# Performance work log

Hardware: AMD Instinct MI355X
Metric: run time of the kernel (lower is better)

Reference implementation:

```python
import jax, jax.numpy as jnp
import numpy as np


def _fft_feats(x):
    # x: [B, 3, H, W] float32
    B, C, H, W = x.shape
    gray = 0.299 * x[:, 0] + 0.587 * x[:, 1] + 0.114 * x[:, 2]  # [B,H,W]
    mag = jnp.abs(jnp.fft.fftshift(jnp.fft.fft2(gray), axes=(-2, -1))) + 1e-8
    mag = mag / (mag.max(axis=(-2, -1), keepdims=True) + 1e-8)
    m = mag.reshape(B, -1)
    n = m.shape[1]
    mean = m.mean(axis=1)
    std = jnp.clip(jnp.std(m, axis=1, ddof=1), 1e-8, None)  # torch unbiased std
    mx = m.max(axis=1)
    mn = m.min(axis=1)
    gt_mean = (m > mean[:, None]).astype(jnp.float32).mean(axis=1)
    # torch.median returns the lower of the two middle values for even n
    med = jnp.sort(m, axis=1)[:, (n - 1) // 2]
    q1 = mag[:, : H // 4].mean(axis=(1, 2))
    q2 = mag[:, H // 4 : H // 2].mean(axis=(1, 2))
    q3 = mag[:, H // 2 : 3 * H // 4].mean(axis=(1, 2))
    q4 = mag[:, 3 * H // 4 :].mean(axis=(1, 2))
    gt_half = (m > 0.5).astype(jnp.float32).mean(axis=1)
    gt_tenth = (m > 0.1).astype(jnp.float32).mean(axis=1)
    feats = jnp.stack([mean, std, mx, mn, gt_mean, med, q1, q2, q3, q4, gt_half, gt_tenth], axis=1)
    return jnp.clip(feats, -10.0, 10.0)  # [B,12]


def _bn(h, gamma, beta):
    # BatchNorm1d, training-mode forward (batch statistics, biased var), eps=1e-5
    mu = h.mean(axis=0)
    var = h.var(axis=0)
    return gamma * (h - mu) / jnp.sqrt(var + 1e-5) + beta


def _mlp(f, W1, b1, g1, be1, W2, b2, g2, be2, W3, b3):
    h = jax.nn.relu(_bn(f @ W1 + b1, g1, be1))  # Dropout(0.1) treated as identity (eval)
    h = jax.nn.relu(_bn(h @ W2 + b2, g2, be2))
    return h @ W3 + b3


def setup_inputs() -> dict:
    key = jax.random.key(0)
    ks = jax.random.split(key, 8)
    B, H, W = 64, 512, 512
    D = 512  # output_dim
    x = jax.random.normal(ks[0], (B, 3, H, W), dtype=jnp.float32)
    W1 = jax.random.normal(ks[1], (12, 64), dtype=jnp.float32) * 0.2
    b1 = jnp.zeros((64,), jnp.float32)
    g1 = jnp.ones((64,), jnp.float32)
    be1 = jnp.zeros((64,), jnp.float32)
    W2 = jax.random.normal(ks[2], (64, 128), dtype=jnp.float32) * 0.1
    b2 = jnp.zeros((128,), jnp.float32)
    g2 = jnp.ones((128,), jnp.float32)
    be2 = jnp.zeros((128,), jnp.float32)
    W3 = jax.random.normal(ks[3], (128, D), dtype=jnp.float32) * 0.08
    b3 = jnp.zeros((D,), jnp.float32)
    return {"x": x, "W1": W1, "b1": b1, "g1": g1, "be1": be1,
            "W2": W2, "b2": b2, "g2": g2, "be2": be2, "W3": W3, "b3": b3}


def reference(x, W1, b1, g1, be1, W2, b2, g2, be2, W3, b3):
    feats = _fft_feats(x)
    return _mlp(feats, W1, b1, g1, be1, W2, b2, g2, be2, W3, b3)
```

## Files before the change

kernel.cpp:

```cpp
#include <hip/hip_runtime.h>
#include <math.h>

#ifndef M_PI
#define M_PI 3.14159265358979323846
#endif

#define BB 64
#define HH 512
#define WW 512
#define NPIX (HH*WW)
#define MED_K 131072u
#define MAGB 131584
#define BSTRIDE 264
#define SS 520

__device__ __forceinline__ float wredf(float v){
  #pragma unroll
  for (int o = 32; o > 0; o >>= 1) v += __shfl_down(v, o, 64);
  return v;
}
__device__ __forceinline__ float wred_min(float v){
  #pragma unroll
  for (int o = 32; o > 0; o >>= 1) v = fminf(v, __shfl_down(v, o, 64));
  return v;
}
__device__ __forceinline__ float wred_max(float v){
  #pragma unroll
  for (int o = 32; o > 0; o >>= 1) v = fmaxf(v, __shfl_down(v, o, 64));
  return v;
}
__device__ __forceinline__ unsigned wred_addu(unsigned v){
  #pragma unroll
  for (int o = 32; o > 0; o >>= 1) v += __shfl_down(v, o, 64);
  return v;
}
__device__ __forceinline__ float wred_add_all(float v){
  #pragma unroll
  for (int o = 32; o > 0; o >>= 1) v += __shfl_xor(v, o, 64);
  return v;
}

__global__ void init_kernel(float2* __restrict__ twg, unsigned* __restrict__ scal){
  int t = threadIdx.x;
  double a = -2.0 * M_PI * (double)t / 512.0;
  twg[t] = make_float2((float)cos(a), (float)sin(a));
  #pragma unroll
  for (int q = 0; q < 8; ++q){
    int w = t*8 + q;
    scal[w] = (w >= 64 && w < 128) ? 0xFFFFFFFFu : 0u;
  }
}

__device__ __forceinline__ void build_twid(float2* T, const float2* __restrict__ twg,
                                           int t, int nthr){
  for (int i = t; i < 510; i += nthr){
    int v = i + 2;
    int z = 31 - __clz(v);
    T[i] = twg[(v - (1 << z)) << (8 - z)];
  }
}

__device__ __forceinline__ void bfly_stage(float (&re)[8], float (&im)[8],
                                           int d, float A, float B, float C, float D){
  #pragma unroll
  for (int r = 0; r < 8; ++r){
    float ore = __shfl_xor(re[r], d, 64);
    float oim = __shfl_xor(im[r], d, 64);
    float sre = re[r], sim = im[r];
    re[r] = A*sre + B*ore + C*sim + D*oim;
    im[r] = A*sim + B*oim - C*sre - D*ore;
  }
}

__device__ __forceinline__ void wave_fft512(float (&re)[8], float (&im)[8],
                                            const float2* T, int lane){
  {
    float A = (lane & 1) ? -1.f : 1.f;
    #pragma unroll
    for (int r = 0; r < 8; ++r){
      float ore = __shfl_xor(re[r], 1, 64);
      float oim = __shfl_xor(im[r], 1, 64);
      re[r] = A*re[r] + ore;
      im[r] = A*im[r] + oim;
    }
  }
  #pragma unroll
  for (int st = 2; st <= 6; ++st){
    const int d = 1 << (st - 1);
    float2 w = T[((1 << (st - 1)) - 2) + (lane & (d - 1))];
    bool hi = (lane & d) != 0;
    float A = hi ? -w.x : 1.f;
    float B = hi ? 1.f : w.x;
    float C = hi ? w.y : 0.f;
    float D = hi ? 0.f : -w.y;
    bfly_stage(re, im, d, A, B, C, D);
  }
  {
    float2 w = T[62 + lane];
    #pragma unroll
    for (int r = 0; r < 8; r += 2){
      float vr = w.x*re[r+1] - w.y*im[r+1];
      float vi = w.x*im[r+1] + w.y*re[r+1];
      float ur = re[r], ui = im[r];
      re[r]   = ur + vr; im[r]   = ui + vi;
      re[r+1] = ur - vr; im[r+1] = ui - vi;
    }
  }
  {
    float2 w0 = T[126 + lane];
    float2 w1 = T[190 + lane];
    #pragma unroll
    for (int rb = 0; rb < 8; rb += 4){
      {
        float vr = w0.x*re[rb+2] - w0.y*im[rb+2];
        float vi = w0.x*im[rb+2] + w0.y*re[rb+2];
        float ur = re[rb], ui = im[rb];
        re[rb]   = ur + vr; im[rb]   = ui + vi;
        re[rb+2] = ur - vr; im[rb+2] = ui - vi;
      }
      {
        float vr = w1.x*re[rb+3] - w1.y*im[rb+3];
        float vi = w1.x*im[rb+3] + w1.y*re[rb+3];
        float ur = re[rb+1], ui = im[rb+1];
        re[rb+1] = ur + vr; im[rb+1] = ui + vi;
        re[rb+3] = ur - vr; im[rb+3] = ui - vi;
      }
    }
  }
  {
    #pragma unroll
    for (int r = 0; r < 4; ++r){
      float2 w = T[254 + 64*r + lane];
      float vr = w.x*re[r+4] - w.y*im[r+4];
      float vi = w.x*im[r+4] + w.y*re[r+4];
      float ur = re[r], ui = im[r];
      re[r]   = ur + vr; im[r]   = ui + vi;
      re[r+4] = ur - vr; im[r+4] = ui - vi;
    }
  }
}

__global__ __launch_bounds__(256) void row_fft_kernel(const float* __restrict__ x,
                                                      const float2* __restrict__ twg,
                                                      float2* __restrict__ out){
  __shared__ float2 T[510];
  int t = threadIdx.x;
  build_twid(T, twg, t, 256);
  __syncthreads();
  int lane = t & 63, wv = t >> 6;
  int pair = blockIdx.x*4 + wv;
  int b = pair >> 8, hp = pair & 255;
  int c0 = lane << 3;
  const float* p0 = x + (size_t)b*3*NPIX + (size_t)(2*hp)*WW + c0;
  const float* p1 = p0 + WW;
  float4 ra0 = *(const float4*)(p0);          float4 ra1 = *(const float4*)(p0+4);
  float4 ga0 = *(const float4*)(p0+NPIX);     float4 ga1 = *(const float4*)(p0+NPIX+4);
  float4 ba0 = *(const float4*)(p0+2*NPIX);   float4 ba1 = *(const float4*)(p0+2*NPIX+4);
  float4 rb0 = *(const float4*)(p1);          float4 rb1 = *(const float4*)(p1+4);
  float4 gb0 = *(const float4*)(p1+NPIX);     float4 gb1 = *(const float4*)(p1+NPIX+4);
  float4 bb0 = *(const float4*)(p1+2*NPIX);   float4 bb1 = *(const float4*)(p1+2*NPIX+4);
  float g0[8] = {0.299f*ra0.x + 0.587f*ga0.x + 0.114f*ba0.x,
                 0.299f*ra0.y + 0.587f*ga0.y + 0.114f*ba0.y,
                 0.299f*ra0.z + 0.587f*ga0.z + 0.114f*ba0.z,
                 0.299f*ra0.w + 0.587f*ga0.w + 0.114f*ba0.w,
                 0.299f*ra1.x + 0.587f*ga1.x + 0.114f*ba1.x,
                 0.299f*ra1.y + 0.587f*ga1.y + 0.114f*ba1.y,
                 0.299f*ra1.z + 0.587f*ga1.z + 0.114f*ba1.z,
                 0.299f*ra1.w + 0.587f*ga1.w + 0.114f*ba1.w};
  float g1[8] = {0.299f*rb0.x + 0.587f*gb0.x + 0.114f*bb0.x,
                 0.299f*rb0.y + 0.587f*gb0.y + 0.114f*bb0.y,
                 0.299f*rb0.z + 0.587f*gb0.z + 0.114f*bb0.z,
                 0.299f*rb0.w + 0.587f*gb0.w + 0.114f*bb0.w,
                 0.299f*rb1.x + 0.587f*gb1.x + 0.114f*bb1.x,
                 0.299f*rb1.y + 0.587f*gb1.y + 0.114f*bb1.y,
                 0.299f*rb1.z + 0.587f*gb1.z + 0.114f*bb1.z,
                 0.299f*rb1.w + 0.587f*gb1.w + 0.114f*bb1.w};
  int src = (int)(__brev((unsigned)lane) >> 26);
  float re[8], im[8];
  re[0] = __shfl(g0[0], src, 64); re[1] = __shfl(g0[4], src, 64);
  re[2] = __shfl(g0[2], src, 64); re[3] = __shfl(g0[6], src, 64);
  re[4] = __shfl(g0[1], src, 64); re[5] = __shfl(g0[5], src, 64);
  re[6] = __shfl(g0[3], src, 64); re[7] = __shfl(g0[7], src, 64);
  im[0] = __shfl(g1[0], src, 64); im[1] = __shfl(g1[4], src, 64);
  im[2] = __shfl(g1[2], src, 64); im[3] = __shfl(g1[6], src, 64);
  im[4] = __shfl(g1[1], src, 64); im[5] = __shfl(g1[5], src, 64);
  im[6] = __shfl(g1[3], src, 64); im[7] = __shfl(g1[7], src, 64);
  wave_fft512(re, im, T, lane);
  int row0 = (b << 9) + 2*hp;
  float2* o0 = out + (size_t)row0*BSTRIDE;
  float2* o1 = o0 + BSTRIDE;
  int srcl = (64 - lane) & 63;
  float p4r = __shfl(re[4], srcl, 64), p4i = __shfl(im[4], srcl, 64);
  float p5r = __shfl(re[5], srcl, 64), p5i = __shfl(im[5], srcl, 64);
  float p6r = __shfl(re[6], srcl, 64), p6i = __shfl(im[6], srcl, 64);
  float p7r = __shfl(re[7], srcl, 64), p7i = __shfl(im[7], srcl, 64);
  bool l0 = (lane == 0);
  {
    float zr = re[0], zi = im[0];
    float wr = l0 ? re[0] : p7r, wi = l0 ? im[0] : p7i;
    o0[lane] = make_float2(0.5f*(zr + wr), 0.5f*(zi - wi));
    o1[lane] = make_float2(0.5f*(zi + wi), 0.5f*(wr - zr));
  }
  {
    float zr = re[1], zi = im[1];
    float wr = l0 ? re[7] : p6r, wi = l0 ? im[7] : p6i;
    int k = lane + 64;
    o0[k] = make_float2(0.5f*(zr + wr), 0.5f*(zi - wi));
    o1[k] = make_float2(0.5f*(zi + wi), 0.5f*(wr - zr));
  }
  {
    float zr = re[2], zi = im[2];
    float wr = l0 ? re[6] : p5r, wi = l0 ? im[6] : p5i;
    int k = lane + 128;
    o0[k] = make_float2(0.5f*(zr + wr), 0.5f*(zi - wi));
    o1[k] = make_float2(0.5f*(zi + wi), 0.5f*(wr - zr));
  }
  {
    float zr = re[3], zi = im[3];
    float wr = l0 ? re[5] : p4r, wi = l0 ? im[5] : p4i;
    int k = lane + 192;
    o0[k] = make_float2(0.5f*(zr + wr), 0.5f*(zi - wi));
    o1[k] = make_float2(0.5f*(zi + wi), 0.5f*(wr - zr));
  }
  if (l0){
    float zr = re[4], zi = im[4];
    o0[256] = make_float2(zr, 0.f);
    o1[256] = make_float2(zi, 0.f);
  }
}

__global__ __launch_bounds__(512) void col_fft_kernel(const float2* __restrict__ in,
    const float2* __restrict__ twg,
    float* __restrict__ magc,
    unsigned* __restrict__ dmax, unsigned* __restrict__ dmin,
    double* __restrict__ sum, double* __restrict__ sumsq, double* __restrict__ qsum,
    unsigned* __restrict__ hist1)
{
  __shared__ float st_re[8*SS];
  __shared__ float st_im[8*SS];
  __shared__ float2 T[510];
  __shared__ unsigned h[8*256];
  __shared__ float buff[8][8];
  int t = threadIdx.x;
  int lane = t & 63, wv = t >> 6;
  build_twid(T, twg, t, 512);
  for (int i = t; i < 2048; i += 512) h[i] = 0u;
  int b = blockIdx.x / 33;
  int j0 = (blockIdx.x % 33) << 3;
  const float2* base = in + (size_t)b * (size_t)(512*BSTRIDE);
  #pragma unroll
  for (int it = 0; it < 8; ++it){
    int idx = t + (it << 9);
    int e = idx >> 3, jj = idx & 7;
    float2 v = base[(size_t)e*BSTRIDE + j0 + jj];
    int se = e ^ (e >> 3);
    st_re[jj*SS + se] = v.x;
    st_im[jj*SS + se] = v.y;
  }
  __syncthreads();
  int j = j0 + wv;
  if (j <= 256){
    int K = (int)(__brev((unsigned)lane) >> 26);
    const int rv3[8] = {0,4,2,6,1,5,3,7};
    float re[8], im[8];
    #pragma unroll
    for (int r = 0; r < 8; ++r){
      int e = 8*K + rv3[r];
      int se = e ^ K;
      re[r] = st_re[wv*SS + se];
      im[r] = st_im[wv*SS + se];
    }
    wave_fft512(re, im, T, lane);
    unsigned wu = (j == 0 || j == 256) ? 1u : 2u;
    float* mo = magc + (size_t)b*MAGB + (size_t)j*512;
    unsigned* hw = h + (wv << 8);
    float lsum=0.f, lsq=0.f;
    float lq[4] = {0.f, 0.f, 0.f, 0.f};
    float lmn = 3.4e38f, lmx = 0.f;
    const int QA[8]  = {2,2,3,3,0,0,1,1};
    const int QBM[8] = {1,1,0,0,3,3,2,2};
    #pragma unroll
    for (int r = 0; r < 8; ++r){
      float m = sqrtf(re[r]*re[r] + im[r]*im[r]) + 1e-8f;
      const int basei = 64*((r+4)&7);
      mo[basei + lane] = m;
      float wm = (wu == 2u) ? m + m : m;
      lsum += wm;
      lsq = fmaf(wm, m, lsq);
      lmn = fminf(lmn, m); lmx = fmaxf(lmx, m);
      atomicAdd(&hw[__float_as_uint(m) >> 23], wu);
      lq[QA[r]] += m;
      if (wu == 2u){
        if ((r & 1) == 0){
          float m0 = (lane == 0) ? m : 0.f;
          lq[QBM[r]] += m - m0;
          lq[(QBM[r]+1)&3] += m0;
        } else {
          lq[QBM[r]] += m;
        }
      }
    }
    float r0 = wredf(lsum), r1 = wredf(lsq);
    float r2 = wredf(lq[0]), r3 = wredf(lq[1]), r4 = wredf(lq[2]), r5 = wredf(lq[3]);
    float fmn = wred_min(lmn), fmx = wred_max(lmx);
    if (lane == 0){
      buff[0][wv]=r0; buff[1][wv]=r1; buff[2][wv]=r2;
      buff[3][wv]=r3; buff[4][wv]=r4; buff[5][wv]=r5;
      buff[6][wv]=fmn; buff[7][wv]=fmx;
    }
  }
  __syncthreads();
  int nact = 257 - j0; if (nact > 8) nact = 8;
  if (t == 0){
    double s0=0,s1=0,s2=0,s3=0,s4=0,s5=0; float mn=3.4e38f, mx=0.f;
    for (int i = 0; i < nact; ++i){
      s0+=(double)buff[0][i]; s1+=(double)buff[1][i]; s2+=(double)buff[2][i];
      s3+=(double)buff[3][i]; s4+=(double)buff[4][i]; s5+=(double)buff[5][i];
      mn=fminf(mn,buff[6][i]); mx=fmaxf(mx,buff[7][i]);
    }
    atomicAdd(sum + b, s0);
    atomicAdd(sumsq + b, s1);
    atomicAdd(qsum + b*4 + 0, s2);
    atomicAdd(qsum + b*4 + 1, s3);
    atomicAdd(qsum + b*4 + 2, s4);
    atomicAdd(qsum + b*4 + 3, s5);
    atomicMin(dmin + b, __float_as_uint(mn));
    atomicMax(dmax + b, __float_as_uint(mx));
  }
  unsigned* hb = hist1 + (size_t)b*256;
  if (t < 256){
    unsigned c = h[t] + h[256+t] + h[512+t] + h[768+t]
               + h[1024+t] + h[1280+t] + h[1536+t] + h[1792+t];
    if (c) atomicAdd(&hb[t], c);
  }
}

__global__ __launch_bounds__(256) void pass2_kernel(const float4* __restrict__ magc4,
    const unsigned* __restrict__ hist1, const double* __restrict__ sum,
    const unsigned* __restrict__ dmax,
    unsigned* __restrict__ hist2, unsigned* __restrict__ cnt_gtm,
    unsigned* __restrict__ cnt_half, unsigned* __restrict__ cnt_tenth)
{
  __shared__ __align__(16) unsigned h[16384];
  __shared__ unsigned part[256];
  __shared__ unsigned rb[3][4];
  __shared__ unsigned s_sel;
  int t = threadIdx.x, b = blockIdx.x;
  {
    uint4 z = make_uint4(0u,0u,0u,0u);
    for (int i = t; i < 4096; i += 256) ((uint4*)h)[i] = z;
  }
  const unsigned* hb1 = hist1 + (size_t)b*256;
  part[t] = hb1[t];
  __syncthreads();
  if (t == 0){
    unsigned target = MED_K, cum = 0; int bin = 0;
    for (; bin < 256; ++bin){ if (cum + part[bin] >= target) break; cum += part[bin]; }
    s_sel = (unsigned)bin;
  }
  __syncthreads();
  unsigned s1 = s_sel;
  float meanf = (float)(sum[b] / (double)NPIX);
  float d = __uint_as_float(dmax[b]) + 1e-8f;
  float th = 0.5f*d, tl = 0.1f*d;
  int c_lo = blockIdx.y * 65;
  int ncols = 257 - c_lo; if (ncols > 65) ncols = 65;
  const float4* p = magc4 + (size_t)b*(MAGB/4) + (size_t)c_lo*128;
  unsigned lgm = 0, lh = 0, lt = 0;
  int n4 = ncols * 128;
  for (int idx = t; idx < n4; idx += 256){
    float4 v = p[idx];
    int col = c_lo + (idx >> 7);
    unsigned w = (col == 0 || col == 256) ? 1u : 2u;
    float a[4] = {v.x, v.y, v.z, v.w};
    #pragma unroll
    for (int q = 0; q < 4; ++q){
      float m = a[q];
      unsigned bits = __float_as_uint(m);
      if ((bits >> 23) == s1) atomicAdd(&h[(bits >> 9) & 0x3fffu], w);
      lgm += (m > meanf) ? w : 0u;
      lh  += (m > th) ? w : 0u;
      lt  += (m > tl) ? w : 0u;
    }
  }
  int lane = t & 63, wv = t >> 6;
  unsigned g0 = wred_addu(lgm), g1 = wred_addu(lh), g2 = wred_addu(lt);
  if (lane == 0){ rb[0][wv]=g0; rb[1][wv]=g1; rb[2][wv]=g2; }
  __syncthreads();
  if (t == 0){
    unsigned a0=0,a1=0,a2=0;
    for (int i = 0; i < 4; ++i){ a0+=rb[0][i]; a1+=rb[1][i]; a2+=rb[2][i]; }
    atomicAdd(cnt_gtm + b, a0);
    atomicAdd(cnt_half + b, a1);
    atomicAdd(cnt_tenth + b, a2);
  }
  unsigned* hb = hist2 + (((size_t)b*4) + blockIdx.y)*16384;
  for (int i = t; i < 4096; i += 256)
    ((uint4*)hb)[i] = ((const uint4*)h)[i];
}

__global__ __launch_bounds__(256) void scan2_feats_kernel(
    const unsigned* __restrict__ hist1, const unsigned* __restrict__ hist2,
    const unsigned* __restrict__ dmax, const unsigned* __restrict__ dmin,
    const double* __restrict__ sum, const double* __restrict__ sumsq,
    const double* __restrict__ qsum,
    const unsigned* __restrict__ cnt_half, const unsigned* __restrict__ cnt_tenth,
    const unsigned* __restrict__ cnt_gtmean,
    float* __restrict__ feats)
{
  int b = blockIdx.x, t = threadIdx.x;
  __shared__ __align__(16) unsigned hsum[16384];
  __shared__ unsigned part[256];
  __shared__ unsigned s_sel, s_rem;
  const uint4* h0 = (const uint4*)(hist2 + (size_t)b*4*16384);
  for (int i = t; i < 4096; i += 256){
    uint4 a = h0[i], c = h0[4096 + i], d2 = h0[8192 + i], e = h0[12288 + i];
    uint4 s;
    s.x = a.x + c.x + d2.x + e.x;
    s.y = a.y + c.y + d2.y + e.y;
    s.z = a.z + c.z + d2.z + e.z;
    s.w = a.w + c.w + d2.w + e.w;
    ((uint4*)hsum)[i] = s;
  }
  const unsigned* hb1 = hist1 + (size_t)b*256;
  part[t] = hb1[t];
  __syncthreads();
  if (t == 0){
    unsigned target = MED_K, cum = 0; int bin = 0;
    for (; bin < 256; ++bin){ if (cum + part[bin] >= target) break; cum += part[bin]; }
    s_sel = (unsigned)bin; s_rem = target - cum;
  }
  __syncthreads();
  {
    unsigned sp = 0;
    int basei = t*64;
    for (int i = 0; i < 64; ++i) sp += hsum[basei + ((i + t) & 63)];
    part[t] = sp;
  }
  __syncthreads();
  if (t == 0){
    unsigned target = s_rem, cum = 0; int seg = 0;
    for (; seg < 256; ++seg){ if (cum + part[seg] >= target) break; cum += part[seg]; }
    unsigned r = target - cum;
    int bin = seg*64;
    for (;; ++bin){ unsigned c = hsum[bin]; if (c >= r) break; r -= c; }
    unsigned medbits = (s_sel << 23) | ((unsigned)bin << 9) | 256u;
    float maxv = __uint_as_float(dmax[b]);
    float dd_f = maxv + 1e-8f;
    double dd = (double)dd_f;
    double n = (double)NPIX;
    double sm = sum[b] / dd;
    double sq = sumsq[b] / (dd*dd);
    double mean = sm / n;
    double var = (sq - sm*sm/n) / (n - 1.0);
    if (var < 0.0) var = 0.0;
    float stdv = (float)sqrt(var);
    if (stdv < 1e-8f) stdv = 1e-8f;
    float f[12];
    f[0] = (float)mean;
    f[1] = stdv;
    f[2] = maxv / dd_f;
    f[3] = __uint_as_float(dmin[b]) / dd_f;
    f[4] = (float)((double)cnt_gtmean[b] / n);
    f[5] = __uint_as_float(medbits) / dd_f;
    f[6] = (float)(qsum[b*4+0] / dd * (1.0/65536.0));
    f[7] = (float)(qsum[b*4+1] / dd * (1.0/65536.0));
    f[8] = (float)(qsum[b*4+2] / dd * (1.0/65536.0));
    f[9] = (float)(qsum[b*4+3] / dd * (1.0/65536.0));
    f[10] = (float)((double)cnt_half[b] / n);
    f[11] = (float)((double)cnt_tenth[b] / n);
    #pragma unroll
    for (int i = 0; i < 12; ++i)
      feats[b*12 + i] = fminf(fmaxf(f[i], -10.f), 10.f);
  }
}

__global__ __launch_bounds__(64) void mlp1_kernel(const float* __restrict__ feats,
    const float* __restrict__ W1, const float* __restrict__ b1,
    const float* __restrict__ g1, const float* __restrict__ be1,
    float* __restrict__ h1t)
{
  int c = blockIdx.x, r = threadIdx.x;
  float acc = b1[c];
  #pragma unroll
  for (int k = 0; k < 12; ++k) acc += feats[r*12 + k] * W1[k*64 + c];
  float mu = wred_add_all(acc) * (1.f/BB);
  float dv = acc - mu;
  float var = wred_add_all(dv*dv) * (1.f/BB);
  float scv = g1[c] / sqrtf(var + 1e-5f);
  float v = dv*scv + be1[c];
  h1t[c*BB + r] = v > 0.f ? v : 0.f;
}

__global__ __launch_bounds__(64) void mlp2_kernel(const float* __restrict__ h1t,
    const float* __restrict__ W2, const float* __restrict__ b2,
    const float* __restrict__ g2, const float* __restrict__ be2,
    float* __restrict__ h2t)
{
  int c = blockIdx.x, r = threadIdx.x;
  float acc = b2[c];
  #pragma unroll 4
  for (int k = 0; k < 64; ++k) acc += h1t[k*BB + r] * W2[k*128 + c];
  float mu = wred_add_all(acc) * (1.f/BB);
  float dv = acc - mu;
  float var = wred_add_all(dv*dv) * (1.f/BB);
  float scv = g2[c] / sqrtf(var + 1e-5f);
  float v = dv*scv + be2[c];
  h2t[c*BB + r] = v > 0.f ? v : 0.f;
}

__global__ __launch_bounds__(256) void mlp3_kernel(const float* __restrict__ h2t,
    const float* __restrict__ W3, const float* __restrict__ b3,
    float* __restrict__ out)
{
  int r = threadIdx.x & 63;
  int w = threadIdx.x >> 6;
  int c = blockIdx.x*4 + w;
  float acc = b3[c];
  #pragma unroll 4
  for (int k = 0; k < 128; ++k) acc += h2t[k*BB + r] * W3[k*512 + c];
  out[r*512 + c] = acc;
}

extern "C" void kernel_launch(void* const* d_in, const int* in_sizes, int n_in,
                              void* d_out, int out_size, void* d_ws, size_t ws_size,
                              hipStream_t stream) {
  (void)in_sizes; (void)n_in; (void)out_size; (void)ws_size;
  const float* x   = (const float*)d_in[0];
  const float* W1  = (const float*)d_in[1];
  const float* b1  = (const float*)d_in[2];
  const float* g1  = (const float*)d_in[3];
  const float* be1 = (const float*)d_in[4];
  const float* W2  = (const float*)d_in[5];
  const float* b2  = (const float*)d_in[6];
  const float* g2  = (const float*)d_in[7];
  const float* be2 = (const float*)d_in[8];
  const float* W3  = (const float*)d_in[9];
  const float* b3  = (const float*)d_in[10];
  float* out = (float*)d_out;

  char* ws = (char*)d_ws;
  float2* bufc = (float2*)ws;
  float*  magc = (float*)(ws + 134217728);
  unsigned* hist1 = (unsigned*)(ws + 134217728 + 34078720);
  unsigned* hist2 = (unsigned*)(ws + 168296448 + 65536);
  char* sc = ws + 168361984 + 16777216;
  unsigned* dmax      = (unsigned*)(sc + 0);
  unsigned* dmin      = (unsigned*)(sc + 256);
  double*   sum       = (double*)(sc + 512);
  double*   sumsq     = (double*)(sc + 1024);
  double*   qsum      = (double*)(sc + 1536);
  unsigned* cnt_half  = (unsigned*)(sc + 3584);
  unsigned* cnt_tenth = (unsigned*)(sc + 3840);
  unsigned* cnt_gtm   = (unsigned*)(sc + 4096);
  float*    feats     = (float*)(sc + 5120);
  float*    h1t       = (float*)(sc + 8192);
  float*    h2t       = (float*)(sc + 8192 + 16384);
  float2*   twg       = (float2*)(sc + 8192 + 16384 + 32768);

  hipMemsetAsync(hist1, 0, 65536, stream);

  init_kernel<<<1, 256, 0, stream>>>(twg, (unsigned*)sc);
  row_fft_kernel<<<BB*64, 256, 0, stream>>>(x, twg, bufc);
  col_fft_kernel<<<BB*33, 512, 0, stream>>>(bufc, twg, magc, dmax, dmin, sum, sumsq, qsum, hist1);
  pass2_kernel<<<dim3(BB, 4), 256, 0, stream>>>((const float4*)magc, hist1, sum, dmax,
      hist2, cnt_gtm, cnt_half, cnt_tenth);
  scan2_feats_kernel<<<BB, 256, 0, stream>>>(hist1, hist2, dmax, dmin, sum, sumsq, qsum,
      cnt_half, cnt_tenth, cnt_gtm, feats);
  mlp1_kernel<<<64, 64, 0, stream>>>(feats, W1, b1, g1, be1, h1t);
  mlp2_kernel<<<128, 64, 0, stream>>>(h1t, W2, b2, g2, be2, h2t);
  mlp3_kernel<<<128, 256, 0, stream>>>(h2t, W3, b3, out);
}
```

Baseline: 441.3 us.

## Widen pass2 grid with halved fine histogram, global atomic merge, fused MLP1/2

Splits the median-refinement pass into 16 column slices per image instead of 4. The shared fine histogram is halved to 8192 bins (one less mantissa bit), and slices merge through global atomics into a single per-image histogram rather than four copies. This shrinks LDS use and the scan kernel's read. The first two MLP layers are fused into one single-block kernel that keeps the hidden activations in shared memory, removing a launch. In exchange it adds a larger memset, atomic contention on the global histogram, and a coarser median bin.

```diff
diff --git a/kernel.cpp b/kernel.cpp
--- a/kernel.cpp
+++ b/kernel.cpp
@@ -13,6 +13,7 @@
 #define MAGB 131584
 #define BSTRIDE 264
 #define SS 520
+#define NFINE 8192
 
 __device__ __forceinline__ float wredf(float v){
   #pragma unroll
@@ -341,14 +342,14 @@
     unsigned* __restrict__ hist2, unsigned* __restrict__ cnt_gtm,
     unsigned* __restrict__ cnt_half, unsigned* __restrict__ cnt_tenth)
 {
-  __shared__ __align__(16) unsigned h[16384];
+  __shared__ __align__(16) unsigned h[NFINE];
   __shared__ unsigned part[256];
   __shared__ unsigned rb[3][4];
   __shared__ unsigned s_sel;
   int t = threadIdx.x, b = blockIdx.x;
   {
     uint4 z = make_uint4(0u,0u,0u,0u);
-    for (int i = t; i < 4096; i += 256) ((uint4*)h)[i] = z;
+    for (int i = t; i < NFINE/4; i += 256) ((uint4*)h)[i] = z;
   }
   const unsigned* hb1 = hist1 + (size_t)b*256;
   part[t] = hb1[t];
@@ -363,8 +364,9 @@
   float meanf = (float)(sum[b] / (double)NPIX);
   float d = __uint_as_float(dmax[b]) + 1e-8f;
   float th = 0.5f*d, tl = 0.1f*d;
-  int c_lo = blockIdx.y * 65;
-  int ncols = 257 - c_lo; if (ncols > 65) ncols = 65;
+  int y = blockIdx.y;
+  int c_lo = (y == 0) ? 0 : 16*y + 1;
+  int ncols = (y == 0) ? 17 : 16;
   const float4* p = magc4 + (size_t)b*(MAGB/4) + (size_t)c_lo*128;
   unsigned lgm = 0, lh = 0, lt = 0;
   int n4 = ncols * 128;
@@ -377,7 +379,7 @@
     for (int q = 0; q < 4; ++q){
       float m = a[q];
       unsigned bits = __float_as_uint(m);
-      if ((bits >> 23) == s1) atomicAdd(&h[(bits >> 9) & 0x3fffu], w);
+      if ((bits >> 23) == s1) atomicAdd(&h[(bits >> 10) & 0x1fffu], w);
       lgm += (m > meanf) ? w : 0u;
       lh  += (m > th) ? w : 0u;
       lt  += (m > tl) ? w : 0u;
@@ -394,9 +396,11 @@
     atomicAdd(cnt_half + b, a1);
     atomicAdd(cnt_tenth + b, a2);
   }
-  unsigned* hb = hist2 + (((size_t)b*4) + blockIdx.y)*16384;
-  for (int i = t; i < 4096; i += 256)
-    ((uint4*)hb)[i] = ((const uint4*)h)[i];
+  unsigned* hb = hist2 + (size_t)b*NFINE;
+  for (int i = t; i < NFINE; i += 256){
+    unsigned c = h[i];
+    if (c) atomicAdd(&hb[i], c);
+  }
 }
 
 __global__ __launch_bounds__(256) void scan2_feats_kernel(
@@ -409,19 +413,12 @@
     float* __restrict__ feats)
 {
   int b = blockIdx.x, t = threadIdx.x;
-  __shared__ __align__(16) unsigned hsum[16384];
+  __shared__ __align__(16) unsigned hsum[NFINE];
   __shared__ unsigned part[256];
   __shared__ unsigned s_sel, s_rem;
-  const uint4* h0 = (const uint4*)(hist2 + (size_t)b*4*16384);
-  for (int i = t; i < 4096; i += 256){
-    uint4 a = h0[i], c = h0[4096 + i], d2 = h0[8192 + i], e = h0[12288 + i];
-    uint4 s;
-    s.x = a.x + c.x + d2.x + e.x;
-    s.y = a.y + c.y + d2.y + e.y;
-    s.z = a.z + c.z + d2.z + e.z;
-    s.w = a.w + c.w + d2.w + e.w;
-    ((uint4*)hsum)[i] = s;
-  }
+  const uint4* h0 = (const uint4*)(hist2 + (size_t)b*NFINE);
+  for (int i = t; i < NFINE/4; i += 256)
+    ((uint4*)hsum)[i] = h0[i];
   const unsigned* hb1 = hist1 + (size_t)b*256;
   part[t] = hb1[t];
   __syncthreads();
@@ -433,8 +430,8 @@
   __syncthreads();
   {
     unsigned sp = 0;
-    int basei = t*64;
-    for (int i = 0; i < 64; ++i) sp += hsum[basei + ((i + t) & 63)];
+    int basei = t*32;
+    for (int i = 0; i < 32; ++i) sp += hsum[basei + ((i + t) & 31)];
     part[t] = sp;
   }
   __syncthreads();
@@ -442,9 +439,9 @@
     unsigned target = s_rem, cum = 0; int seg = 0;
     for (; seg < 256; ++seg){ if (cum + part[seg] >= target) break; cum += part[seg]; }
     unsigned r = target - cum;
-    int bin = seg*64;
+    int bin = seg*32;
     for (;; ++bin){ unsigned c = hsum[bin]; if (c >= r) break; r -= c; }
-    unsigned medbits = (s_sel << 23) | ((unsigned)bin << 9) | 256u;
+    unsigned medbits = (s_sel << 23) | ((unsigned)bin << 10) | 512u;
     float maxv = __uint_as_float(dmax[b]);
     float dd_f = maxv + 1e-8f;
     double dd = (double)dd_f;
@@ -475,38 +472,45 @@
   }
 }
 
-__global__ __launch_bounds__(64) void mlp1_kernel(const float* __restrict__ feats,
+__global__ __launch_bounds__(512) void mlp12_kernel(const float* __restrict__ feats,
     const float* __restrict__ W1, const float* __restrict__ b1,
     const float* __restrict__ g1, const float* __restrict__ be1,
-    float* __restrict__ h1t)
-{
-  int c = blockIdx.x, r = threadIdx.x;
-  float acc = b1[c];
-  #pragma unroll
-  for (int k = 0; k < 12; ++k) acc += feats[r*12 + k] * W1[k*64 + c];
-  float mu = wred_add_all(acc) * (1.f/BB);
-  float dv = acc - mu;
-  float var = wred_add_all(dv*dv) * (1.f/BB);
-  float scv = g1[c] / sqrtf(var + 1e-5f);
-  float v = dv*scv + be1[c];
-  h1t[c*BB + r] = v > 0.f ? v : 0.f;
-}
-
-__global__ __launch_bounds__(64) void mlp2_kernel(const float* __restrict__ h1t,
     const float* __restrict__ W2, const float* __restrict__ b2,
     const float* __restrict__ g2, const float* __restrict__ be2,
     float* __restrict__ h2t)
 {
-  int c = blockIdx.x, r = threadIdx.x;
-  float acc = b2[c];
-  #pragma unroll 4
-  for (int k = 0; k < 64; ++k) acc += h1t[k*BB + r] * W2[k*128 + c];
-  float mu = wred_add_all(acc) * (1.f/BB);
-  float dv = acc - mu;
-  float var = wred_add_all(dv*dv) * (1.f/BB);
-  float scv = g2[c] / sqrtf(var + 1e-5f);
-  float v = dv*scv + be2[c];
-  h2t[c*BB + r] = v > 0.f ? v : 0.f;
+  __shared__ float h1[64*64];
+  int t = threadIdx.x, lane = t & 63, wv = t >> 6;
+  float f[12];
+  #pragma unroll
+  for (int k = 0; k < 12; ++k) f[k] = feats[lane*12 + k];
+  #pragma unroll
+  for (int i = 0; i < 8; ++i){
+    int c = wv*8 + i;
+    float acc = b1[c];
+    #pragma unroll
+    for (int k = 0; k < 12; ++k) acc += f[k] * W1[k*64 + c];
+    float mu = wred_add_all(acc) * (1.f/BB);
+    float dv = acc - mu;
+    float var = wred_add_all(dv*dv) * (1.f/BB);
+    float scv = g1[c] / sqrtf(var + 1e-5f);
+    float v = dv*scv + be1[c];
+    h1[c*64 + lane] = v > 0.f ? v : 0.f;
+  }
+  __syncthreads();
+  #pragma unroll
+  for (int i = 0; i < 16; ++i){
+    int c = wv*16 + i;
+    float acc = b2[c];
+    #pragma unroll 4
+    for (int k = 0; k < 64; ++k) acc += h1[k*64 + lane] * W2[k*128 + c];
+    float mu = wred_add_all(acc) * (1.f/BB);
+    float dv = acc - mu;
+    float var = wred_add_all(dv*dv) * (1.f/BB);
+    float scv = g2[c] / sqrtf(var + 1e-5f);
+    float v = dv*scv + be2[c];
+    h2t[c*BB + lane] = v > 0.f ? v : 0.f;
+  }
 }
 
 __global__ __launch_bounds__(256) void mlp3_kernel(const float* __restrict__ h2t,
@@ -544,7 +548,7 @@
   float*  magc = (float*)(ws + 134217728);
   unsigned* hist1 = (unsigned*)(ws + 134217728 + 34078720);
   unsigned* hist2 = (unsigned*)(ws + 168296448 + 65536);
-  char* sc = ws + 168361984 + 16777216;
+  char* sc = ws + 168361984 + 2097152;
   unsigned* dmax      = (unsigned*)(sc + 0);
   unsigned* dmin      = (unsigned*)(sc + 256);
   double*   sum       = (double*)(sc + 512);
@@ -554,20 +558,18 @@
   unsigned* cnt_tenth = (unsigned*)(sc + 3840);
   unsigned* cnt_gtm   = (unsigned*)(sc + 4096);
   float*    feats     = (float*)(sc + 5120);
-  float*    h1t       = (float*)(sc + 8192);
-  float*    h2t       = (float*)(sc + 8192 + 16384);
-  float2*   twg       = (float2*)(sc + 8192 + 16384 + 32768);
-
-  hipMemsetAsync(hist1, 0, 65536, stream);
+  float*    h2t       = (float*)(sc + 8192);
+  float2*   twg       = (float2*)(sc + 8192 + 32768);
+
+  hipMemsetAsync(hist1, 0, 65536 + 2097152, stream);
 
   init_kernel<<<1, 256, 0, stream>>>(twg, (unsigned*)sc);
   row_fft_kernel<<<BB*64, 256, 0, stream>>>(x, twg, bufc);
   col_fft_kernel<<<BB*33, 512, 0, stream>>>(bufc, twg, magc, dmax, dmin, sum, sumsq, qsum, hist1);
-  pass2_kernel<<<dim3(BB, 4), 256, 0, stream>>>((const float4*)magc, hist1, sum, dmax,
+  pass2_kernel<<<dim3(BB, 16), 256, 0, stream>>>((const float4*)magc, hist1, sum, dmax,
       hist2, cnt_gtm, cnt_half, cnt_tenth);
   scan2_feats_kernel<<<BB, 256, 0, stream>>>(hist1, hist2, dmax, dmin, sum, sumsq, qsum,
       cnt_half, cnt_tenth, cnt_gtm, feats);
-  mlp1_kernel<<<64, 64, 0, stream>>>(feats, W1, b1, g1, be1, h1t);
-  mlp2_kernel<<<128, 64, 0, stream>>>(h1t, W2, b2, g2, be2, h2t);
+  mlp12_kernel<<<1, 512, 0, stream>>>(feats, W1, b1, g1, be1, W2, b2, g2, be2, h2t);
   mlp3_kernel<<<128, 256, 0, stream>>>(h2t, W3, b3, out);
 }
```

Measured after the change: 483.9 us. 9.7% more time.
